# Kernel optimization log

Measured on AMD Instinct MI355X. Metric: run time of the kernel, lower is better.

## Reference

```python
import jax, jax.numpy as jnp
import numpy as np

B, H, L, D = 2, 16, 1024, 64
R, E = 16, 4  # num_relations, rank


def setup_inputs() -> dict:
    key = jax.random.key(0)
    k1, k2, k3, k4, k5 = jax.random.split(key, 5)
    Q = jax.random.normal(k1, (B, H, L, D), jnp.float32)
    K = jax.random.normal(k2, (B, H, L, D), jnp.float32)
    relation_ids = jax.random.randint(k3, (B, L, L), 0, R, jnp.int32)
    # Original inits A1/A2 to zeros (identity A); use small random values so the
    # low-rank relation-specific term is exercised nontrivially.
    A1 = jax.random.normal(k4, (R, H, D, E), jnp.float32) * 0.02
    A2 = jax.random.normal(k5, (R, H, E, D), jnp.float32) * 0.02
    return {"Q": Q, "K": K, "relation_ids": relation_ids, "A1": A1, "A2": A2}


def reference(Q, K, relation_ids, A1, A2):
    # A_r = A1_r @ A2_r + I, so score[b,h,l,m] = Q.K^T + (Q A1_r)(A2_r K^T)
    # with r = relation_ids[b,l,m]. Entries whose relation id is outside
    # [0, R) are never accumulated in the original loop -> masked to 0.
    num_rel = A1.shape[0]
    rank = A1.shape[-1]
    base = jnp.einsum('bhld,bhmd->bhlm', Q, K)                 # identity part
    u = jnp.einsum('bhld,rhde->bhlre', Q, A1)                  # (B,H,L,R,E) small
    v = jnp.einsum('bhmd,rhed->bhmre', K, A2)                  # (B,H,M,R,E) small
    idx = jnp.clip(relation_ids, 0, num_rel - 1)
    # gather per-(l,m) relation's query projection: (B,H,L,L,E)
    ug = jnp.take_along_axis(u, idx[:, None, :, :, None], axis=3)
    # gather per-(l,m) relation's key projection: (B,H,L,M,E)
    vg = jnp.take_along_axis(v[:, :, None], idx[:, None, :, :, None, None], axis=4)[..., 0, :]
    low = jnp.sum(ug * vg, axis=-1)
    valid = ((relation_ids >= 0) & (relation_ids < num_rel))[:, None]
    return (base + low) * valid.astype(base.dtype)
```

## Files before the change

kernel.cpp:

```cpp
#include <hip/hip_runtime.h>
#include <hip/hip_bf16.h>
#include <stdint.h>

#define Bsz 2
#define Hn  16
#define Ln  1024
#define Dn  64
#define Rn  16
#define En  4

typedef short short8 __attribute__((ext_vector_type(8)));
typedef float f32x4  __attribute__((ext_vector_type(4)));

__device__ __forceinline__ unsigned short f32_to_bf16_rne(float f) {
    union { float f; uint32_t u; } x; x.f = f;
    uint32_t u = x.u;
    u += 0x7FFFu + ((u >> 16) & 1u);
    return (unsigned short)(u >> 16);
}

__global__ __launch_bounds__(256) void uv_kernel(
    const float* __restrict__ Q, const float* __restrict__ K,
    const float* __restrict__ A1, const float* __restrict__ A2,
    float* __restrict__ ws_u, float* __restrict__ ws_v)
{
    __shared__ float Xs[16 * 68];
    __shared__ float Ah[16 * 65 * 4];

    const int tid = threadIdx.x;
    const int bh  = blockIdx.y;
    const int h   = bh & 15;
    const int l0  = blockIdx.x * 16;
    const int isV = blockIdx.z;

    const float* X = (isV ? K : Q) + (size_t)bh * Ln * Dn;

    {
        const int row = tid >> 4, c4 = tid & 15;
        const float4 v = *(const float4*)&X[(size_t)(l0 + row) * Dn + c4 * 4];
        *(float4*)&Xs[row * 68 + c4 * 4] = v;
    }
    if (!isV) {
        #pragma unroll
        for (int i = 0; i < 4; ++i) {
            const int p = tid + i * 256;
            const int r = p >> 6, d = p & 63;
            const float4 v = *(const float4*)&A1[(((size_t)r * Hn + h) * Dn + d) * En];
            *(float4*)&Ah[(r * 65 + d) * 4] = v;
        }
    } else {
        #pragma unroll
        for (int i = 0; i < 4; ++i) {
            const int p = tid + i * 256;
            const int r = p >> 6, d = p & 63;
            float4 v;
            v.x = A2[(((size_t)r * Hn + h) * En + 0) * Dn + d];
            v.y = A2[(((size_t)r * Hn + h) * En + 1) * Dn + d];
            v.z = A2[(((size_t)r * Hn + h) * En + 2) * Dn + d];
            v.w = A2[(((size_t)r * Hn + h) * En + 3) * Dn + d];
            *(float4*)&Ah[(r * 65 + d) * 4] = v;
        }
    }
    __syncthreads();

    const int li = tid >> 4, r = tid & 15;
    float ax = 0.f, ay = 0.f, az = 0.f, aw = 0.f;
    #pragma unroll
    for (int d = 0; d < Dn; ++d) {
        const float x = Xs[li * 68 + d];
        const float4 a = *(const float4*)&Ah[(r * 65 + d) * 4];
        ax += x * a.x; ay += x * a.y; az += x * a.z; aw += x * a.w;
    }
    float* dst = (isV ? ws_v : ws_u);
    float4 o; o.x = ax; o.y = ay; o.z = az; o.w = aw;
    *(float4*)&dst[((size_t)bh * Ln + l0 + li) * 64 + r * 4] = o;
}

__global__ __launch_bounds__(256) void score_kernel(
    const float* __restrict__ Q, const float* __restrict__ K,
    const int* __restrict__ rid,
    const float* __restrict__ ws_u, const float* __restrict__ ws_v,
    float* __restrict__ out)
{
    __shared__ unsigned short Qs[64 * 72];
    __shared__ unsigned short Ks[64 * 72];
    __shared__ float us[64 * 68];
    __shared__ float vs[64 * 68];

    const int tid = threadIdx.x;
    const int bh  = blockIdx.z;
    const int b   = bh >> 4;
    const int m0  = blockIdx.x * 64;
    const int l0  = blockIdx.y * 64;

    const size_t qkBase = (size_t)bh * Ln * Dn;
    const size_t uvBase = (size_t)bh * Ln * 64;

    #pragma unroll
    for (int i = 0; i < 4; ++i) {
        const int p = tid + i * 256;
        const int row = p >> 4, c4 = p & 15;
        const float4 q = *(const float4*)&Q[qkBase + (size_t)(l0 + row) * Dn + c4 * 4];
        const float4 k = *(const float4*)&K[qkBase + (size_t)(m0 + row) * Dn + c4 * 4];
        ushort4 qb, kb;
        qb.x = f32_to_bf16_rne(q.x); qb.y = f32_to_bf16_rne(q.y);
        qb.z = f32_to_bf16_rne(q.z); qb.w = f32_to_bf16_rne(q.w);
        kb.x = f32_to_bf16_rne(k.x); kb.y = f32_to_bf16_rne(k.y);
        kb.z = f32_to_bf16_rne(k.z); kb.w = f32_to_bf16_rne(k.w);
        *(ushort4*)&Qs[row * 72 + c4 * 4] = qb;
        *(ushort4*)&Ks[row * 72 + c4 * 4] = kb;
        const float4 u = *(const float4*)&ws_u[uvBase + (size_t)(l0 + row) * 64 + c4 * 4];
        const float4 v = *(const float4*)&ws_v[uvBase + (size_t)(m0 + row) * 64 + c4 * 4];
        *(float4*)&us[row * 68 + c4 * 4] = u;
        *(float4*)&vs[row * 68 + c4 * 4] = v;
    }
    __syncthreads();

    const int w    = tid >> 6;
    const int lane = tid & 63;
    const int quad = lane >> 4;
    const int ln   = lane & 15;

    f32x4 acc[4];
    #pragma unroll
    for (int t = 0; t < 4; ++t) { f32x4 z = {0.f, 0.f, 0.f, 0.f}; acc[t] = z; }

    #pragma unroll
    for (int s = 0; s < 2; ++s) {
        const short8 aF = *(const short8*)&Qs[(w * 16 + ln) * 72 + s * 32 + quad * 8];
        #pragma unroll
        for (int t = 0; t < 4; ++t) {
            const short8 bF = *(const short8*)&Ks[(t * 16 + ln) * 72 + s * 32 + quad * 8];
            acc[t] = __builtin_amdgcn_mfma_f32_16x16x32_bf16(aF, bF, acc[t], 0, 0, 0);
        }
    }

    #pragma unroll
    for (int t = 0; t < 4; ++t) {
        const int m_local = t * 16 + ln;
        const int m = m0 + m_local;
        #pragma unroll
        for (int reg = 0; reg < 4; ++reg) {
            const int l_local = w * 16 + quad * 4 + reg;
            const int l = l0 + l_local;
            const int rv = rid[((size_t)b * Ln + l) * Ln + m];
            const bool valid = (rv >= 0) && (rv < Rn);
            const int r = valid ? rv : 0;
            const float4 uu = *(const float4*)&us[l_local * 68 + r * 4];
            const float4 vv = *(const float4*)&vs[m_local * 68 + r * 4];
            const float low = uu.x * vv.x + uu.y * vv.y + uu.z * vv.z + uu.w * vv.w;
            const float res = valid ? (acc[t][reg] + low) : 0.f;
            out[((size_t)bh * Ln + l) * Ln + m] = res;
        }
    }
}

extern "C" void kernel_launch(void* const* d_in, const int* in_sizes, int n_in,
                              void* d_out, int out_size, void* d_ws, size_t ws_size,
                              hipStream_t stream) {
    const float* Q   = (const float*)d_in[0];
    const float* K   = (const float*)d_in[1];
    const int*   rid = (const int*)d_in[2];
    const float* A1  = (const float*)d_in[3];
    const float* A2  = (const float*)d_in[4];
    float* out = (float*)d_out;

    float* ws_u = (float*)d_ws;
    float* ws_v = ws_u + (size_t)Bsz * Hn * Ln * 64;

    uv_kernel<<<dim3(Ln / 16, Bsz * Hn, 2), 256, 0, stream>>>(Q, K, A1, A2, ws_u, ws_v);
    score_kernel<<<dim3(Ln / 64, Ln / 64, Bsz * Hn), 256, 0, stream>>>(Q, K, rid, ws_u, ws_v, out);
}
```

Before: 214.8 us.

## Store u/v projections in bf16, prefetch relation ids, use nontemporal output stores

The u/v low-rank projections are written and read as bf16 instead of fp32, halving that workspace traffic and the shared-memory footprint of the score kernel. Relation ids are loaded into registers at kernel start so their global-load latency overlaps the Q/K staging. Output uses nontemporal stores, and launch bounds request 4 blocks per CU. The bf16 rounding of u/v adds small numerical error to the low-rank term.

```diff
diff --git a/kernel.cpp b/kernel.cpp
--- a/kernel.cpp
+++ b/kernel.cpp
@@ -19,10 +19,15 @@
     return (unsigned short)(u >> 16);
 }
 
+__device__ __forceinline__ float bf16_to_f32(unsigned short s) {
+    union { uint32_t u; float f; } x; x.u = ((uint32_t)s) << 16;
+    return x.f;
+}
+
 __global__ __launch_bounds__(256) void uv_kernel(
     const float* __restrict__ Q, const float* __restrict__ K,
     const float* __restrict__ A1, const float* __restrict__ A2,
-    float* __restrict__ ws_u, float* __restrict__ ws_v)
+    unsigned short* __restrict__ ws_u, unsigned short* __restrict__ ws_v)
 {
     __shared__ float Xs[16 * 68];
     __shared__ float Ah[16 * 65 * 4];
@@ -71,21 +76,23 @@
         const float4 a = *(const float4*)&Ah[(r * 65 + d) * 4];
         ax += x * a.x; ay += x * a.y; az += x * a.z; aw += x * a.w;
     }
-    float* dst = (isV ? ws_v : ws_u);
-    float4 o; o.x = ax; o.y = ay; o.z = az; o.w = aw;
-    *(float4*)&dst[((size_t)bh * Ln + l0 + li) * 64 + r * 4] = o;
+    unsigned short* dst = (isV ? ws_v : ws_u);
+    ushort4 o;
+    o.x = f32_to_bf16_rne(ax); o.y = f32_to_bf16_rne(ay);
+    o.z = f32_to_bf16_rne(az); o.w = f32_to_bf16_rne(aw);
+    *(ushort4*)&dst[((size_t)bh * Ln + l0 + li) * 64 + r * 4] = o;
 }
 
-__global__ __launch_bounds__(256) void score_kernel(
+__global__ __launch_bounds__(256, 4) void score_kernel(
     const float* __restrict__ Q, const float* __restrict__ K,
     const int* __restrict__ rid,
-    const float* __restrict__ ws_u, const float* __restrict__ ws_v,
+    const unsigned short* __restrict__ ws_u, const unsigned short* __restrict__ ws_v,
     float* __restrict__ out)
 {
     __shared__ unsigned short Qs[64 * 72];
     __shared__ unsigned short Ks[64 * 72];
-    __shared__ float us[64 * 68];
-    __shared__ float vs[64 * 68];
+    __shared__ unsigned short us[64 * 68];
+    __shared__ unsigned short vs[64 * 68];
 
     const int tid = threadIdx.x;
     const int bh  = blockIdx.z;
@@ -93,8 +100,23 @@
     const int m0  = blockIdx.x * 64;
     const int l0  = blockIdx.y * 64;
 
+    const int w    = tid >> 6;
+    const int lane = tid & 63;
+    const int quad = lane >> 4;
+    const int ln   = lane & 15;
+
     const size_t qkBase = (size_t)bh * Ln * Dn;
     const size_t uvBase = (size_t)bh * Ln * 64;
+
+    int ridv[16];
+    {
+        const size_t ridRow0 = ((size_t)b * Ln + l0 + w * 16 + quad * 4) * Ln + m0 + ln;
+        #pragma unroll
+        for (int t = 0; t < 4; ++t)
+            #pragma unroll
+            for (int reg = 0; reg < 4; ++reg)
+                ridv[t * 4 + reg] = rid[ridRow0 + (size_t)reg * Ln + t * 16];
+    }
 
     #pragma unroll
     for (int i = 0; i < 4; ++i) {
@@ -109,17 +131,12 @@
         kb.z = f32_to_bf16_rne(k.z); kb.w = f32_to_bf16_rne(k.w);
         *(ushort4*)&Qs[row * 72 + c4 * 4] = qb;
         *(ushort4*)&Ks[row * 72 + c4 * 4] = kb;
-        const float4 u = *(const float4*)&ws_u[uvBase + (size_t)(l0 + row) * 64 + c4 * 4];
-        const float4 v = *(const float4*)&ws_v[uvBase + (size_t)(m0 + row) * 64 + c4 * 4];
-        *(float4*)&us[row * 68 + c4 * 4] = u;
-        *(float4*)&vs[row * 68 + c4 * 4] = v;
+        const ushort4 u = *(const ushort4*)&ws_u[uvBase + (size_t)(l0 + row) * 64 + c4 * 4];
+        const ushort4 v = *(const ushort4*)&ws_v[uvBase + (size_t)(m0 + row) * 64 + c4 * 4];
+        *(ushort4*)&us[row * 68 + c4 * 4] = u;
+        *(ushort4*)&vs[row * 68 + c4 * 4] = v;
     }
     __syncthreads();
-
-    const int w    = tid >> 6;
-    const int lane = tid & 63;
-    const int quad = lane >> 4;
-    const int ln   = lane & 15;
 
     f32x4 acc[4];
     #pragma unroll
@@ -143,14 +160,17 @@
         for (int reg = 0; reg < 4; ++reg) {
             const int l_local = w * 16 + quad * 4 + reg;
             const int l = l0 + l_local;
-            const int rv = rid[((size_t)b * Ln + l) * Ln + m];
+            const int rv = ridv[t * 4 + reg];
             const bool valid = (rv >= 0) && (rv < Rn);
             const int r = valid ? rv : 0;
-            const float4 uu = *(const float4*)&us[l_local * 68 + r * 4];
-            const float4 vv = *(const float4*)&vs[m_local * 68 + r * 4];
-            const float low = uu.x * vv.x + uu.y * vv.y + uu.z * vv.z + uu.w * vv.w;
+            const ushort4 uu = *(const ushort4*)&us[l_local * 68 + r * 4];
+            const ushort4 vv = *(const ushort4*)&vs[m_local * 68 + r * 4];
+            const float low = bf16_to_f32(uu.x) * bf16_to_f32(vv.x)
+                            + bf16_to_f32(uu.y) * bf16_to_f32(vv.y)
+                            + bf16_to_f32(uu.z) * bf16_to_f32(vv.z)
+                            + bf16_to_f32(uu.w) * bf16_to_f32(vv.w);
             const float res = valid ? (acc[t][reg] + low) : 0.f;
-            out[((size_t)bh * Ln + l) * Ln + m] = res;
+            __builtin_nontemporal_store(res, &out[((size_t)bh * Ln + l) * Ln + m]);
         }
     }
 }
@@ -165,8 +185,8 @@
     const float* A2  = (const float*)d_in[4];
     float* out = (float*)d_out;
 
-    float* ws_u = (float*)d_ws;
-    float* ws_v = ws_u + (size_t)Bsz * Hn * Ln * 64;
+    unsigned short* ws_u = (unsigned short*)d_ws;
+    unsigned short* ws_v = ws_u + (size_t)Bsz * Hn * Ln * 64;
 
     uv_kernel<<<dim3(Ln / 16, Bsz * Hn, 2), 256, 0, stream>>>(Q, K, A1, A2, ws_u, ws_v);
     score_kernel<<<dim3(Ln / 64, Ln / 64, Bsz * Hn), 256, 0, stream>>>(Q, K, rid, ws_u, ws_v, out);
```

Result: faster. 200.7 us (-6.5%).
